# Performance work log

Measured on AMD Instinct MI355X. Metric: run time of the kernel, lower is better.

## Reference

```python
import jax, jax.numpy as jnp
import numpy as np
import math

CAPACITY_FACTOR = 1.25
MIN_CAPACITY = 4


def _get_capacity(num_tokens, num_experts):
    capacity = math.floor(CAPACITY_FACTOR * num_tokens / num_experts)
    capacity += capacity % 2  # make even
    return max(capacity, MIN_CAPACITY)


def setup_inputs() -> dict:
    key = jax.random.key(0)
    s, e = 16384, 8
    inputs = jax.random.normal(key, (s, e), dtype=jnp.float32)
    return {"inputs": inputs}


def reference(inputs):
    s, num_experts = inputs.shape
    capacity = _get_capacity(s, num_experts)  # static: 2560

    # autocast_softmax: softmax in fp32
    logits = jax.nn.softmax(inputs.astype(jnp.float32), axis=-1)  # [s, e]

    top1_idx = jnp.argmax(inputs, axis=-1)  # [s]
    mask = jax.nn.one_hot(top1_idx, num_experts, dtype=jnp.int32)  # [s, e]

    # moe_cumsum: exclusive position of each token within its expert queue
    ranks = jnp.cumsum(mask, axis=0) - 1  # [s, e]
    # 'first' select policy: drop tokens beyond capacity
    mask = mask * (ranks < capacity).astype(jnp.int32)  # [s, e]
    ranks = jnp.sum(mask * ranks, axis=-1)  # [s] position within assigned expert

    ranks_oh = jax.nn.one_hot(ranks, capacity, dtype=logits.dtype)  # [s, c]
    weight = mask.astype(logits.dtype) * logits  # [s, e]
    combine_weights = weight[:, :, None] * ranks_oh[:, None, :]  # [s, e, c]
    sec_mask = combine_weights.astype(bool)
    return combine_weights, sec_mask
```

## Files before the change

kernel.cpp:

```cpp
#include <hip/hip_runtime.h>
#include <cstdint>

#define S_TOKENS 16384
#define NEXP     8
#define CAP      2560
#define BLK      256
#define NBLK     (S_TOKENS / BLK)
#define NWAVE    (BLK / 64)

__global__ __launch_bounds__(BLK) void k_route(const float* __restrict__ in,
                                               float* __restrict__ prob,
                                               int* __restrict__ packed,
                                               int* __restrict__ block_counts) {
    int t = blockIdx.x * BLK + threadIdx.x;
    const float4* p4 = reinterpret_cast<const float4*>(in + (size_t)t * NEXP);
    float4 a = p4[0], b = p4[1];
    float x[8] = {a.x, a.y, a.z, a.w, b.x, b.y, b.z, b.w};

    float m = x[0]; int idx = 0;
#pragma unroll
    for (int i = 1; i < 8; ++i) {
        if (x[i] > m) { m = x[i]; idx = i; }
    }
    float s = 0.f;
#pragma unroll
    for (int i = 0; i < 8; ++i) s += __expf(x[i] - m);
    float p = 1.0f / s;

    unsigned long long bal[NEXP];
#pragma unroll
    for (int e = 0; e < NEXP; ++e) bal[e] = __ballot(idx == e);

    int lane = threadIdx.x & 63;
    int wv   = threadIdx.x >> 6;

    __shared__ int wcnt[NWAVE][NEXP];
    if (lane < NEXP) wcnt[wv][lane] = __popcll(bal[lane]);
    __syncthreads();

    unsigned long long ltmask = (1ULL << lane) - 1ULL;
    int r = __popcll(bal[idx] & ltmask);
#pragma unroll
    for (int w = 0; w < NWAVE; ++w)
        if (w < wv) r += wcnt[w][idx];

    prob[t]   = p;
    packed[t] = (r << 3) | idx;

    if (threadIdx.x < NEXP) {
        int c = 0;
#pragma unroll
        for (int w = 0; w < NWAVE; ++w) c += wcnt[w][threadIdx.x];
        block_counts[blockIdx.x * NEXP + threadIdx.x] = c;
    }
}

__global__ void k_scan(const int* __restrict__ block_counts,
                       int* __restrict__ block_offs) {
    int e = threadIdx.x;
    if (e < NEXP) {
        int acc = 0;
        for (int b = 0; b < NBLK; ++b) {
            block_offs[b * NEXP + e] = acc;
            acc += block_counts[b * NEXP + e];
        }
    }
}

__global__ __launch_bounds__(BLK) void k_scatter(const float* __restrict__ prob,
                                                 const int* __restrict__ packed,
                                                 const int* __restrict__ block_offs,
                                                 float* __restrict__ out,
                                                 size_t mask_base) {
    int t = blockIdx.x * BLK + threadIdx.x;
    int pk  = packed[t];
    int idx = pk & 7;
    int r   = pk >> 3;
    int g = block_offs[blockIdx.x * NEXP + idx] + r;
    if (g < CAP) {
        size_t o = ((size_t)t * NEXP + idx) * CAP + (size_t)g;
        out[o] = prob[t];
        out[mask_base + o] = 1.0f;
    }
}

extern "C" void kernel_launch(void* const* d_in, const int* in_sizes, int n_in,
                              void* d_out, int out_size, void* d_ws, size_t ws_size,
                              hipStream_t stream) {
    const float* in = (const float*)d_in[0];
    float* out = (float*)d_out;

    char* ws = (char*)d_ws;
    float* prob   = (float*)(ws);
    int*   packed = (int*)(ws + (64 << 10));
    int*   bcnt   = (int*)(ws + (128 << 10));
    int*   boff   = (int*)(ws + (130 << 10));

    hipMemsetAsync(d_out, 0, (size_t)out_size * sizeof(float), stream);

    k_route<<<NBLK, BLK, 0, stream>>>(in, prob, packed, bcnt);
    k_scan<<<1, 64, 0, stream>>>(bcnt, boff);

    size_t mask_base = (size_t)out_size / 2;
    k_scatter<<<NBLK, BLK, 0, stream>>>(prob, packed, boff, out, mask_base);
}
```

Baseline: 437.1 us.

## Fuse output zero-fill with routing kernel and fold block scan into scatter

```diff
diff --git a/kernel.cpp b/kernel.cpp
--- a/kernel.cpp
+++ b/kernel.cpp
@@ -7,76 +7,84 @@
 #define BLK      256
 #define NBLK     (S_TOKENS / BLK)
 #define NWAVE    (BLK / 64)
+#define FILL_BLOCKS 2048
 
-__global__ __launch_bounds__(BLK) void k_route(const float* __restrict__ in,
-                                               float* __restrict__ prob,
-                                               int* __restrict__ packed,
-                                               int* __restrict__ block_counts) {
-    int t = blockIdx.x * BLK + threadIdx.x;
-    const float4* p4 = reinterpret_cast<const float4*>(in + (size_t)t * NEXP);
-    float4 a = p4[0], b = p4[1];
-    float x[8] = {a.x, a.y, a.z, a.w, b.x, b.y, b.z, b.w};
+typedef unsigned int u32x4 __attribute__((ext_vector_type(4)));
 
-    float m = x[0]; int idx = 0;
+__global__ __launch_bounds__(BLK) void k_fill_route(const float* __restrict__ in,
+                                                    float* __restrict__ prob,
+                                                    int* __restrict__ packed,
+                                                    int* __restrict__ block_counts,
+                                                    u32x4* __restrict__ out4,
+                                                    long n4) {
+    if (blockIdx.x < NBLK) {
+        int t = blockIdx.x * BLK + threadIdx.x;
+        const float4* p4 = reinterpret_cast<const float4*>(in + (size_t)t * NEXP);
+        float4 a = p4[0], b = p4[1];
+        float x[8] = {a.x, a.y, a.z, a.w, b.x, b.y, b.z, b.w};
+
+        float m = x[0]; int idx = 0;
 #pragma unroll
-    for (int i = 1; i < 8; ++i) {
-        if (x[i] > m) { m = x[i]; idx = i; }
+        for (int i = 1; i < 8; ++i) {
+            if (x[i] > m) { m = x[i]; idx = i; }
+        }
+        float s = 0.f;
+#pragma unroll
+        for (int i = 0; i < 8; ++i) s += __expf(x[i] - m);
+        float p = 1.0f / s;
+
+        unsigned long long bal[NEXP];
+#pragma unroll
+        for (int e = 0; e < NEXP; ++e) bal[e] = __ballot(idx == e);
+
+        int lane = threadIdx.x & 63;
+        int wv   = threadIdx.x >> 6;
+
+        __shared__ int wcnt[NWAVE][NEXP];
+        if (lane < NEXP) wcnt[wv][lane] = __popcll(bal[lane]);
+        __syncthreads();
+
+        unsigned long long ltmask = (1ULL << lane) - 1ULL;
+        int r = __popcll(bal[idx] & ltmask);
+#pragma unroll
+        for (int w = 0; w < NWAVE; ++w)
+            if (w < wv) r += wcnt[w][idx];
+
+        prob[t]   = p;
+        packed[t] = (r << 3) | idx;
+
+        if (threadIdx.x < NEXP) {
+            int c = 0;
+#pragma unroll
+            for (int w = 0; w < NWAVE; ++w) c += wcnt[w][threadIdx.x];
+            block_counts[blockIdx.x * NEXP + threadIdx.x] = c;
+        }
     }
-    float s = 0.f;
-#pragma unroll
-    for (int i = 0; i < 8; ++i) s += __expf(x[i] - m);
-    float p = 1.0f / s;
 
-    unsigned long long bal[NEXP];
-#pragma unroll
-    for (int e = 0; e < NEXP; ++e) bal[e] = __ballot(idx == e);
-
-    int lane = threadIdx.x & 63;
-    int wv   = threadIdx.x >> 6;
-
-    __shared__ int wcnt[NWAVE][NEXP];
-    if (lane < NEXP) wcnt[wv][lane] = __popcll(bal[lane]);
-    __syncthreads();
-
-    unsigned long long ltmask = (1ULL << lane) - 1ULL;
-    int r = __popcll(bal[idx] & ltmask);
-#pragma unroll
-    for (int w = 0; w < NWAVE; ++w)
-        if (w < wv) r += wcnt[w][idx];
-
-    prob[t]   = p;
-    packed[t] = (r << 3) | idx;
-
-    if (threadIdx.x < NEXP) {
-        int c = 0;
-#pragma unroll
-        for (int w = 0; w < NWAVE; ++w) c += wcnt[w][threadIdx.x];
-        block_counts[blockIdx.x * NEXP + threadIdx.x] = c;
-    }
-}
-
-__global__ void k_scan(const int* __restrict__ block_counts,
-                       int* __restrict__ block_offs) {
-    int e = threadIdx.x;
-    if (e < NEXP) {
-        int acc = 0;
-        for (int b = 0; b < NBLK; ++b) {
-            block_offs[b * NEXP + e] = acc;
-            acc += block_counts[b * NEXP + e];
-        }
+    u32x4 z = (u32x4)(0u);
+    long stride = (long)gridDim.x * (long)blockDim.x;
+    for (long i = (long)blockIdx.x * BLK + threadIdx.x; i < n4; i += stride) {
+        __builtin_nontemporal_store(z, &out4[i]);
     }
 }
 
 __global__ __launch_bounds__(BLK) void k_scatter(const float* __restrict__ prob,
                                                  const int* __restrict__ packed,
-                                                 const int* __restrict__ block_offs,
+                                                 const int* __restrict__ block_counts,
                                                  float* __restrict__ out,
                                                  size_t mask_base) {
+    __shared__ int sb[NBLK * NEXP];
+    for (int i = threadIdx.x; i < NBLK * NEXP; i += BLK)
+        sb[i] = block_counts[i];
+    __syncthreads();
+
     int t = blockIdx.x * BLK + threadIdx.x;
     int pk  = packed[t];
     int idx = pk & 7;
-    int r   = pk >> 3;
-    int g = block_offs[blockIdx.x * NEXP + idx] + r;
+    int g   = pk >> 3;
+    for (int b = 0; b < blockIdx.x; ++b)
+        g += sb[b * NEXP + idx];
+
     if (g < CAP) {
         size_t o = ((size_t)t * NEXP + idx) * CAP + (size_t)g;
         out[o] = prob[t];
@@ -94,13 +102,12 @@
     float* prob   = (float*)(ws);
     int*   packed = (int*)(ws + (64 << 10));
     int*   bcnt   = (int*)(ws + (128 << 10));
-    int*   boff   = (int*)(ws + (130 << 10));
 
-    hipMemsetAsync(d_out, 0, (size_t)out_size * sizeof(float), stream);
+    long n4 = (long)out_size / 4;
 
-    k_route<<<NBLK, BLK, 0, stream>>>(in, prob, packed, bcnt);
-    k_scan<<<1, 64, 0, stream>>>(bcnt, boff);
+    k_fill_route<<<FILL_BLOCKS, BLK, 0, stream>>>(in, prob, packed, bcnt,
+                                                  (u32x4*)out, n4);
 
     size_t mask_base = (size_t)out_size / 2;
-    k_scatter<<<NBLK, BLK, 0, stream>>>(prob, packed, boff, out, mask_base);
+    k_scatter<<<NBLK, BLK, 0, stream>>>(prob, packed, bcnt, out, mask_base);
 }
```

Result: slower. 604.3 us (+38.2%).
